# Optimization experiments

Hardware: AMD Instinct MI355X
Metric: run time of the kernel (lower is better)

Reference implementation:

```python
import jax, jax.numpy as jnp
import numpy as np

D_GAUSS = 5
N_GAUSS = 100
IN_DIM = 768
T = 100000
LN_EPS = 1e-5


def setup_inputs() -> dict:
    key = jax.random.key(0)
    kx, kw, kb, kc = jax.random.split(key, 4)
    x = jax.random.normal(kx, (T, IN_DIM), dtype=jnp.float32)
    # nn.Linear(input_dim, gaussian_dim)
    lim = 1.0 / np.sqrt(IN_DIM)
    W = jax.random.uniform(kw, (D_GAUSS, IN_DIM), minval=-lim, maxval=lim, dtype=jnp.float32)
    b = jax.random.uniform(kb, (D_GAUSS,), minval=-lim, maxval=lim, dtype=jnp.float32)
    # GM centers (random init, as in GMLayer)
    centers = jax.random.normal(kc, (N_GAUSS, D_GAUSS), dtype=jnp.float32)
    # covariance init exactly as in Gaussian_Layer.__init__: isotropic,
    # scale = (mean nearest-neighbor center distance / 2)^2
    c_np = np.asarray(centers, dtype=np.float64)
    dist = np.sqrt(((c_np[:, None, :] - c_np[None, :, :]) ** 2).sum(-1))
    np.fill_diagonal(dist, np.inf)
    scale = (dist.min(axis=1).mean() / 2.0) ** 2
    cov = np.broadcast_to(np.eye(D_GAUSS) * scale, (N_GAUSS, D_GAUSS, D_GAUSS)).copy()
    covariance = jnp.asarray(cov, dtype=jnp.float32)
    gamma = jnp.ones((N_GAUSS,), dtype=jnp.float32)
    beta = jnp.zeros((N_GAUSS,), dtype=jnp.float32)
    return {"x": x, "W": W, "b": b, "centers": centers,
            "covariance": covariance, "gamma": gamma, "beta": beta}


def reference(x, W, b, centers, covariance, gamma, beta):
    # Linear + Sigmoid projection: [T, d]
    z = jax.nn.sigmoid(x @ W.T + b)
    # Gaussian mixture likelihood per gaussian: [T, K]
    inv_cov = jnp.linalg.inv(covariance)                      # [K, d, d]
    sign, logdet = jnp.linalg.slogdet(covariance)             # [K]
    diff = z[:, None, :] - centers[None, :, :]                # [T, K, d]
    maha = jnp.einsum('tki,kij,tkj->tk', diff, inv_cov, diff)  # [T, K]
    d = centers.shape[-1]
    log2pi = jnp.log(jnp.asarray(2.0 * np.pi, dtype=z.dtype))
    lik = jnp.exp(-0.5 * (maha + d * log2pi + logdet[None, :]))  # [T, K]
    # LayerNorm over the n_gaussians axis
    mu = lik.mean(axis=-1, keepdims=True)
    var = jnp.mean((lik - mu) ** 2, axis=-1, keepdims=True)
    normed = (lik - mu) * jax.lax.rsqrt(var + LN_EPS) * gamma + beta
    # MeanLayer over instances, then squeeze(0): output [K]
    return normed.mean(axis=0)
```

## Files before the change

### kernel.cpp

```cpp
#include <hip/hip_runtime.h>
#include <math.h>

#define D_G 5
#define N_G 100
#define IN_DIM 768
#define T_ROWS 100000
#define LN_EPS 1e-5f

__global__ void precompute_gauss(const float* __restrict__ cov,
                                 float* __restrict__ coeffs) {
    int k = blockIdx.x * blockDim.x + threadIdx.x;
    if (k >= N_G) return;
    double a[D_G][D_G], inv[D_G][D_G];
    for (int i = 0; i < D_G; ++i)
        for (int j = 0; j < D_G; ++j) {
            a[i][j] = (double)cov[(k * D_G + i) * D_G + j];
            inv[i][j] = (i == j) ? 1.0 : 0.0;
        }
    double det = 1.0;
    for (int c = 0; c < D_G; ++c) {
        int p = c;
        double best = fabs(a[c][c]);
        for (int r = c + 1; r < D_G; ++r) {
            double v = fabs(a[r][c]);
            if (v > best) { best = v; p = r; }
        }
        if (p != c) {
            for (int j = 0; j < D_G; ++j) {
                double t = a[c][j]; a[c][j] = a[p][j]; a[p][j] = t;
                t = inv[c][j]; inv[c][j] = inv[p][j]; inv[p][j] = t;
            }
        }
        double piv = a[c][c];
        det *= piv;
        double ip = 1.0 / piv;
        for (int j = 0; j < D_G; ++j) { a[c][j] *= ip; inv[c][j] *= ip; }
        for (int r = 0; r < D_G; ++r) {
            if (r == c) continue;
            double f = a[r][c];
            if (f != 0.0)
                for (int j = 0; j < D_G; ++j) {
                    a[r][j] -= f * a[c][j];
                    inv[r][j] -= f * inv[c][j];
                }
        }
    }
    double logdet = log(fabs(det));
    float* o = coeffs + k * 16;
    for (int i = 0; i < D_G; ++i) o[i] = (float)inv[i][i];
    int idx = D_G;
    for (int i = 0; i < D_G; ++i)
        for (int j = i + 1; j < D_G; ++j) o[idx++] = (float)(2.0 * inv[i][j]);
    o[15] = (float)(-0.5 * ((double)D_G * log(2.0 * 3.14159265358979323846) + logdet));
}

__device__ __forceinline__ float gm_eval(const float z[D_G], const float* ct,
                                         const float* cf, float cc) {
    float d0 = z[0] - ct[0];
    float d1 = z[1] - ct[1];
    float d2 = z[2] - ct[2];
    float d3 = z[3] - ct[3];
    float d4 = z[4] - ct[4];
    float m = cf[0] * (d0 * d0);
    m = fmaf(cf[1], d1 * d1, m);
    m = fmaf(cf[2], d2 * d2, m);
    m = fmaf(cf[3], d3 * d3, m);
    m = fmaf(cf[4], d4 * d4, m);
    m = fmaf(cf[5], d0 * d1, m);
    m = fmaf(cf[6], d0 * d2, m);
    m = fmaf(cf[7], d0 * d3, m);
    m = fmaf(cf[8], d0 * d4, m);
    m = fmaf(cf[9], d1 * d2, m);
    m = fmaf(cf[10], d1 * d3, m);
    m = fmaf(cf[11], d1 * d4, m);
    m = fmaf(cf[12], d2 * d3, m);
    m = fmaf(cf[13], d2 * d4, m);
    m = fmaf(cf[14], d3 * d4, m);
    return __expf(fmaf(-0.5f, m, cc));
}

__launch_bounds__(256)
__global__ void gm_main(const float* __restrict__ x, const float* __restrict__ W,
                        const float* __restrict__ bb,
                        const float* __restrict__ centers,
                        const float* __restrict__ gamma_,
                        const float* __restrict__ beta_,
                        const float* __restrict__ coeffs,
                        float* __restrict__ partials, int nblk) {
    const int lane = threadIdx.x & 63;
    const int wid = threadIdx.x >> 6;
    const int gw = blockIdx.x * 4 + wid;
    const int nw = nblk * 4;

    float4 wreg[D_G][3];
#pragma unroll
    for (int j = 0; j < D_G; ++j)
#pragma unroll
        for (int i = 0; i < 3; ++i)
            wreg[j][i] = *reinterpret_cast<const float4*>(W + j * IN_DIM + i * 256 + lane * 4);

    float bj[D_G];
#pragma unroll
    for (int j = 0; j < D_G; ++j) bj[j] = bb[j];

    const int k0 = lane;
    const bool has1 = lane < (N_G - 64);
    const int k1 = has1 ? (64 + lane) : lane;

    float cf0[15], cf1[15], ct0[D_G], ct1[D_G];
#pragma unroll
    for (int i = 0; i < 15; ++i) { cf0[i] = coeffs[k0 * 16 + i]; cf1[i] = coeffs[k1 * 16 + i]; }
#pragma unroll
    for (int i = 0; i < D_G; ++i) { ct0[i] = centers[k0 * D_G + i]; ct1[i] = centers[k1 * D_G + i]; }
    const float cc0 = coeffs[k0 * 16 + 15], cc1 = coeffs[k1 * 16 + 15];
    const float g0 = gamma_[k0], g1 = gamma_[k1];
    const float be0 = beta_[k0], be1 = beta_[k1];

    float acc0 = 0.f, acc1 = 0.f;

    for (int t = gw; t < T_ROWS; t += nw) {
        const float* xr = x + (size_t)t * IN_DIM;
        const float4 xv0 = *reinterpret_cast<const float4*>(xr + lane * 4);
        const float4 xv1 = *reinterpret_cast<const float4*>(xr + 256 + lane * 4);
        const float4 xv2 = *reinterpret_cast<const float4*>(xr + 512 + lane * 4);

        float p[D_G];
#pragma unroll
        for (int j = 0; j < D_G; ++j) {
            const float4 w0 = wreg[j][0], w1 = wreg[j][1], w2 = wreg[j][2];
            float s = xv0.x * w0.x;
            s = fmaf(xv0.y, w0.y, s);
            s = fmaf(xv0.z, w0.z, s);
            s = fmaf(xv0.w, w0.w, s);
            s = fmaf(xv1.x, w1.x, s);
            s = fmaf(xv1.y, w1.y, s);
            s = fmaf(xv1.z, w1.z, s);
            s = fmaf(xv1.w, w1.w, s);
            s = fmaf(xv2.x, w2.x, s);
            s = fmaf(xv2.y, w2.y, s);
            s = fmaf(xv2.z, w2.z, s);
            s = fmaf(xv2.w, w2.w, s);
            p[j] = s;
        }
#pragma unroll
        for (int j = 0; j < D_G; ++j) {
#pragma unroll
            for (int m = 32; m >= 1; m >>= 1) p[j] += __shfl_xor(p[j], m, 64);
        }
        float z[D_G];
#pragma unroll
        for (int j = 0; j < D_G; ++j)
            z[j] = 1.0f / (1.0f + __expf(-(p[j] + bj[j])));

        const float lik0 = gm_eval(z, ct0, cf0, cc0);
        const float lik1 = has1 ? gm_eval(z, ct1, cf1, cc1) : 0.f;

        float s = lik0 + lik1;
        float q = fmaf(lik0, lik0, lik1 * lik1);
#pragma unroll
        for (int m = 32; m >= 1; m >>= 1) {
            s += __shfl_xor(s, m, 64);
            q += __shfl_xor(q, m, 64);
        }
        const float mu = s * (1.0f / N_G);
        float var = fmaf(q, 1.0f / N_G, -mu * mu);
        var = fmaxf(var, 0.f);
        const float r = rsqrtf(var + LN_EPS);
        acc0 += fmaf((lik0 - mu) * r, g0, be0);
        if (has1) acc1 += fmaf((lik1 - mu) * r, g1, be1);
    }

    __shared__ float sacc[N_G];
    if (threadIdx.x < N_G) sacc[threadIdx.x] = 0.f;
    __syncthreads();
    atomicAdd(&sacc[k0], acc0);
    if (has1) atomicAdd(&sacc[k1], acc1);
    __syncthreads();
    if (threadIdx.x < N_G)
        partials[(size_t)threadIdx.x * nblk + blockIdx.x] = sacc[threadIdx.x];
}

__global__ void reduce_partials(const float* __restrict__ partials,
                                float* __restrict__ out, int nblk) {
    const int k = blockIdx.x;
    const int lane = threadIdx.x & 63;
    const int wid = threadIdx.x >> 6;
    double d = 0.0;
    for (int b = threadIdx.x; b < nblk; b += blockDim.x)
        d += (double)partials[(size_t)k * nblk + b];
#pragma unroll
    for (int m = 32; m >= 1; m >>= 1) d += __shfl_xor(d, m, 64);
    __shared__ double sd[4];
    if (lane == 0) sd[wid] = d;
    __syncthreads();
    if (threadIdx.x == 0)
        out[k] = (float)((sd[0] + sd[1] + sd[2] + sd[3]) * (1.0 / (double)T_ROWS));
}

extern "C" void kernel_launch(void* const* d_in, const int* in_sizes, int n_in,
                              void* d_out, int out_size, void* d_ws, size_t ws_size,
                              hipStream_t stream) {
    const float* x = (const float*)d_in[0];
    const float* W = (const float*)d_in[1];
    const float* b = (const float*)d_in[2];
    const float* centers = (const float*)d_in[3];
    const float* cov = (const float*)d_in[4];
    const float* gamma_ = (const float*)d_in[5];
    const float* beta_ = (const float*)d_in[6];
    float* out = (float*)d_out;

    float* ws = (float*)d_ws;
    float* coeffs = ws;
    float* partials = ws + N_G * 16;

    int nblk = 1024;
    {
        long avail = (long)(ws_size / sizeof(float)) - (long)(N_G * 16);
        long maxblk = avail / N_G;
        if (maxblk < nblk) nblk = (int)maxblk;
        if (nblk < 1) nblk = 1;
    }

    precompute_gauss<<<1, 128, 0, stream>>>(cov, coeffs);
    gm_main<<<nblk, 256, 0, stream>>>(x, W, b, centers, gamma_, beta_, coeffs,
                                      partials, nblk);
    reduce_partials<<<N_G, 256, 0, stream>>>(partials, out, nblk);
}
```

Measured before the change: 447.4 us.

## Prefetch next row of x and hoist gamma/beta out of per-row accumulation

```diff
diff --git a/kernel.cpp b/kernel.cpp
--- a/kernel.cpp
+++ b/kernel.cpp
@@ -30,6 +30,7 @@
                 double t = a[c][j]; a[c][j] = a[p][j]; a[p][j] = t;
                 t = inv[c][j]; inv[c][j] = inv[p][j]; inv[p][j] = t;
             }
+            det = -det;
         }
         double piv = a[c][c];
         det *= piv;
@@ -83,8 +84,6 @@
 __global__ void gm_main(const float* __restrict__ x, const float* __restrict__ W,
                         const float* __restrict__ bb,
                         const float* __restrict__ centers,
-                        const float* __restrict__ gamma_,
-                        const float* __restrict__ beta_,
                         const float* __restrict__ coeffs,
                         float* __restrict__ partials, int nblk) {
     const int lane = threadIdx.x & 63;
@@ -113,33 +112,44 @@
 #pragma unroll
     for (int i = 0; i < D_G; ++i) { ct0[i] = centers[k0 * D_G + i]; ct1[i] = centers[k1 * D_G + i]; }
     const float cc0 = coeffs[k0 * 16 + 15], cc1 = coeffs[k1 * 16 + 15];
-    const float g0 = gamma_[k0], g1 = gamma_[k1];
-    const float be0 = beta_[k0], be1 = beta_[k1];
-
-    float acc0 = 0.f, acc1 = 0.f;
-
-    for (int t = gw; t < T_ROWS; t += nw) {
-        const float* xr = x + (size_t)t * IN_DIM;
-        const float4 xv0 = *reinterpret_cast<const float4*>(xr + lane * 4);
-        const float4 xv1 = *reinterpret_cast<const float4*>(xr + 256 + lane * 4);
-        const float4 xv2 = *reinterpret_cast<const float4*>(xr + 512 + lane * 4);
+
+    float acc0 = 0.f, acc1 = 0.f, accA = 0.f;
+
+    int t = gw;
+    float4 a0{}, a1{}, a2{};
+    if (t < T_ROWS) {
+        const float* xr = x + (size_t)t * IN_DIM + lane * 4;
+        a0 = *reinterpret_cast<const float4*>(xr);
+        a1 = *reinterpret_cast<const float4*>(xr + 256);
+        a2 = *reinterpret_cast<const float4*>(xr + 512);
+    }
+
+    while (t < T_ROWS) {
+        const int tn = t + nw;
+        float4 b0{}, b1{}, b2{};
+        if (tn < T_ROWS) {
+            const float* xr = x + (size_t)tn * IN_DIM + lane * 4;
+            b0 = *reinterpret_cast<const float4*>(xr);
+            b1 = *reinterpret_cast<const float4*>(xr + 256);
+            b2 = *reinterpret_cast<const float4*>(xr + 512);
+        }
 
         float p[D_G];
 #pragma unroll
         for (int j = 0; j < D_G; ++j) {
             const float4 w0 = wreg[j][0], w1 = wreg[j][1], w2 = wreg[j][2];
-            float s = xv0.x * w0.x;
-            s = fmaf(xv0.y, w0.y, s);
-            s = fmaf(xv0.z, w0.z, s);
-            s = fmaf(xv0.w, w0.w, s);
-            s = fmaf(xv1.x, w1.x, s);
-            s = fmaf(xv1.y, w1.y, s);
-            s = fmaf(xv1.z, w1.z, s);
-            s = fmaf(xv1.w, w1.w, s);
-            s = fmaf(xv2.x, w2.x, s);
-            s = fmaf(xv2.y, w2.y, s);
-            s = fmaf(xv2.z, w2.z, s);
-            s = fmaf(xv2.w, w2.w, s);
+            float s = a0.x * w0.x;
+            s = fmaf(a0.y, w0.y, s);
+            s = fmaf(a0.z, w0.z, s);
+            s = fmaf(a0.w, w0.w, s);
+            s = fmaf(a1.x, w1.x, s);
+            s = fmaf(a1.y, w1.y, s);
+            s = fmaf(a1.z, w1.z, s);
+            s = fmaf(a1.w, w1.w, s);
+            s = fmaf(a2.x, w2.x, s);
+            s = fmaf(a2.y, w2.y, s);
+            s = fmaf(a2.z, w2.z, s);
+            s = fmaf(a2.w, w2.w, s);
             p[j] = s;
         }
 #pragma unroll
@@ -166,35 +176,51 @@
         float var = fmaf(q, 1.0f / N_G, -mu * mu);
         var = fmaxf(var, 0.f);
         const float r = rsqrtf(var + LN_EPS);
-        acc0 += fmaf((lik0 - mu) * r, g0, be0);
-        if (has1) acc1 += fmaf((lik1 - mu) * r, g1, be1);
-    }
-
-    __shared__ float sacc[N_G];
-    if (threadIdx.x < N_G) sacc[threadIdx.x] = 0.f;
+        acc0 = fmaf(lik0, r, acc0);
+        if (has1) acc1 = fmaf(lik1, r, acc1);
+        accA = fmaf(mu, r, accA);
+
+        a0 = b0; a1 = b1; a2 = b2;
+        t = tn;
+    }
+
+    __shared__ float sacc[N_G + 1];
+    if (threadIdx.x < N_G + 1) sacc[threadIdx.x] = 0.f;
     __syncthreads();
     atomicAdd(&sacc[k0], acc0);
     if (has1) atomicAdd(&sacc[k1], acc1);
+    if (lane == 0) atomicAdd(&sacc[N_G], accA);
     __syncthreads();
-    if (threadIdx.x < N_G)
+    if (threadIdx.x < N_G + 1)
         partials[(size_t)threadIdx.x * nblk + blockIdx.x] = sacc[threadIdx.x];
 }
 
 __global__ void reduce_partials(const float* __restrict__ partials,
+                                const float* __restrict__ gamma_,
+                                const float* __restrict__ beta_,
                                 float* __restrict__ out, int nblk) {
     const int k = blockIdx.x;
     const int lane = threadIdx.x & 63;
     const int wid = threadIdx.x >> 6;
-    double d = 0.0;
-    for (int b = threadIdx.x; b < nblk; b += blockDim.x)
-        d += (double)partials[(size_t)k * nblk + b];
-#pragma unroll
-    for (int m = 32; m >= 1; m >>= 1) d += __shfl_xor(d, m, 64);
-    __shared__ double sd[4];
-    if (lane == 0) sd[wid] = d;
+    double dk = 0.0, dA = 0.0;
+    for (int b = threadIdx.x; b < nblk; b += blockDim.x) {
+        dk += (double)partials[(size_t)k * nblk + b];
+        dA += (double)partials[(size_t)N_G * nblk + b];
+    }
+#pragma unroll
+    for (int m = 32; m >= 1; m >>= 1) {
+        dk += __shfl_xor(dk, m, 64);
+        dA += __shfl_xor(dA, m, 64);
+    }
+    __shared__ double sk[4], sA[4];
+    if (lane == 0) { sk[wid] = dk; sA[wid] = dA; }
     __syncthreads();
-    if (threadIdx.x == 0)
-        out[k] = (float)((sd[0] + sd[1] + sd[2] + sd[3]) * (1.0 / (double)T_ROWS));
+    if (threadIdx.x == 0) {
+        double S = sk[0] + sk[1] + sk[2] + sk[3];
+        double A = sA[0] + sA[1] + sA[2] + sA[3];
+        out[k] = (float)((double)gamma_[k] * (S - A) * (1.0 / (double)T_ROWS)
+                         + (double)beta_[k]);
+    }
 }
 
 extern "C" void kernel_launch(void* const* d_in, const int* in_sizes, int n_in,
@@ -216,13 +242,12 @@
     int nblk = 1024;
     {
         long avail = (long)(ws_size / sizeof(float)) - (long)(N_G * 16);
-        long maxblk = avail / N_G;
+        long maxblk = avail / (N_G + 1);
         if (maxblk < nblk) nblk = (int)maxblk;
         if (nblk < 1) nblk = 1;
     }
 
     precompute_gauss<<<1, 128, 0, stream>>>(cov, coeffs);
-    gm_main<<<nblk, 256, 0, stream>>>(x, W, b, centers, gamma_, beta_, coeffs,
-                                      partials, nblk);
-    reduce_partials<<<N_G, 256, 0, stream>>>(partials, out, nblk);
-}
+    gm_main<<<nblk, 256, 0, stream>>>(x, W, b, centers, coeffs, partials, nblk);
+    reduce_partials<<<N_G, 256, 0, stream>>>(partials, gamma_, beta_, out, nblk);
+}
```

Result: no change. 438.8 us (-1.9%).
